# Kernel tuning notes

Hardware: AMD Instinct MI355X
Metric: run time of the kernel (lower is better)

Reference implementation:

```python
import jax, jax.numpy as jnp
import numpy as np

B, K, DIM, T_FRAMES = 4, 200, 256, 800

def _conv1d_same(x, w, b):
    # x: [B, K, Cin], w: [3, Cin, Cout] (WIO), 'same' padding over token axis
    y = jax.lax.conv_general_dilated(x, w, window_strides=(1,), padding='SAME',
                                     dimension_numbers=('NWC', 'WIO', 'NWC'))
    return y + b

def _swish_block(x, w1, b1, w2, b2):
    x = jax.nn.silu(x @ w1 + b1)
    return jax.nn.silu(x @ w2 + b2)

def setup_inputs() -> dict:
    key = jax.random.key(0)
    ks = jax.random.split(key, 10)
    def lin(k, fan_in, shape):
        return jax.random.normal(k, shape, dtype=jnp.float32) / np.sqrt(fan_in)
    inp = {
        'T': T_FRAMES,
        'durations': jax.random.uniform(ks[0], (B, K), dtype=jnp.float32) * 4.0,
        'features': jax.random.normal(ks[1], (B, K, DIM), dtype=jnp.float32),
        'conv1_w': lin(ks[2], 3 * DIM, (3, DIM, 8)),
        'conv1_b': jnp.zeros((8,), jnp.float32),
        'conv2_w': lin(ks[3], 3 * DIM, (3, DIM, 8)),
        'conv2_b': jnp.zeros((8,), jnp.float32),
        'sw1_w1': lin(ks[4], 10, (10, 16)), 'sw1_b1': jnp.zeros((16,), jnp.float32),
        'sw1_w2': lin(ks[5], 16, (16, 16)), 'sw1_b2': jnp.zeros((16,), jnp.float32),
        'sw2_w1': lin(ks[6], 10, (10, 2)), 'sw2_b1': jnp.zeros((2,), jnp.float32),
        'sw2_w2': lin(ks[7], 2, (2, 2)), 'sw2_b2': jnp.zeros((2,), jnp.float32),
        'p1_w': lin(ks[8], 2, (2, 1)), 'p1_b': jnp.zeros((1,), jnp.float32),
        'p2_w': lin(ks[9], 16, (16, DIM)), 'p2_b': jnp.zeros((DIM,), jnp.float32),
    }
    return inp

def reference(T, durations, features, conv1_w, conv1_b, conv2_w, conv2_b,
              sw1_w1, sw1_b1, sw1_w2, sw1_b2, sw2_w1, sw2_b1, sw2_w2, sw2_b2,
              p1_w, p1_b, p2_w, p2_b):
    # Conv + SiLU token feature extraction: [B, K, 8]
    left = jax.nn.silu(_conv1d_same(features, conv1_w, conv1_b))
    right = jax.nn.silu(_conv1d_same(features, conv2_w, conv2_b))
    # Token boundary grids S, E: [B, T, K]
    token_end = jnp.cumsum(durations, axis=1)          # [B, K]
    token_start = token_end - durations                # [B, K]
    t = jnp.arange(T, dtype=features.dtype)            # frame index grid
    S = t[None, :, None] - token_start[:, None, :]     # [B, T, K]
    E = token_end[:, None, :] - t[None, :, None]       # [B, T, K]
    Bn, Tn, Kn = S.shape
    # Concat (S, E, conv_feats) -> [B, T, K, 10]
    xleft = jnp.concatenate([S[..., None], E[..., None],
                             jnp.broadcast_to(left[:, None], (Bn, Tn, Kn, 8))], axis=-1)
    xright = jnp.concatenate([S[..., None], E[..., None],
                              jnp.broadcast_to(right[:, None], (Bn, Tn, Kn, 8))], axis=-1)
    C = _swish_block(xleft, sw1_w1, sw1_b1, sw1_w2, sw1_b2)      # [B, T, K, 16]
    r = _swish_block(xright, sw2_w1, sw2_b1, sw2_w2, sw2_b2)     # [B, T, K, 2]
    logits = (r @ p1_w + p1_b)[..., 0]                           # [B, T, K]
    W = jax.nn.softmax(logits, axis=-1)                          # attention over tokens
    # Upsampled output: weighted token features + projected auxiliary context
    O = jnp.einsum('btk,bkd->btd', W, features)
    A = jnp.einsum('btk,btkp->btp', W, C)                        # [B, T, 16]
    return O + (A @ p2_w + p2_b)
```

## Files before the change

### kernel.cpp

```cpp
#include <hip/hip_runtime.h>
#include <math.h>

#define B_   4
#define K_   200
#define DIM_ 256
#define T_   800
#define TT_  4

__device__ __forceinline__ float silu_f(float x) {
    return x / (1.0f + __expf(-x));
}

__global__ __launch_bounds__(64) void prep_kernel(
        const float* __restrict__ dur,
        const float* __restrict__ feats,
        const float* __restrict__ c1w, const float* __restrict__ c1b,
        const float* __restrict__ c2w, const float* __restrict__ c2b,
        float* __restrict__ starts, float* __restrict__ ends,
        float* __restrict__ left,   float* __restrict__ right) {
    const int b = blockIdx.y, chunk = blockIdx.x, k0 = chunk * 4;
    const int tid = threadIdx.x;

    __shared__ float wT[16][772];
    __shared__ float fT[6][260];

    for (int i = tid; i < 3 * DIM_ * 8; i += 64) {
        int tc = i >> 3, o = i & 7;
        wT[o][tc]     = c1w[i];
        wT[8 + o][tc] = c2w[i];
    }
    const float4* f4 = (const float4*)feats;
    for (int i = tid; i < 6 * 64; i += 64) {
        int r = i >> 6, c4 = i & 63;
        int kk = k0 - 1 + r;
        float4 v = make_float4(0.f, 0.f, 0.f, 0.f);
        if (kk >= 0 && kk < K_) v = f4[(b * K_ + kk) * 64 + c4];
        *(float4*)&fT[r][c4 * 4] = v;
    }
    __syncthreads();

    const int k = tid >> 4, oc = tid & 15, cv = oc >> 3, o = oc & 7;
    float acc = 0.f;
#pragma unroll
    for (int tap = 0; tap < 3; ++tap) {
#pragma unroll 8
        for (int c = 0; c < DIM_; c += 4) {
            float4 fv = *(const float4*)&fT[k + tap][c];
            float4 wv = *(const float4*)&wT[oc][tap * DIM_ + c];
            acc += fv.x * wv.x + fv.y * wv.y + fv.z * wv.z + fv.w * wv.w;
        }
    }
    int kk = k0 + k;
    if (kk < K_) {
        float bias = cv ? c2b[o] : c1b[o];
        float* dst = cv ? right : left;
        dst[(b * K_ + kk) * 8 + o] = silu_f(acc + bias);
    }

    if (chunk == 0) {
        float4 dv = make_float4(0.f, 0.f, 0.f, 0.f);
        if (tid < 50) dv = *(const float4*)&dur[b * K_ + tid * 4];
        float s0 = dv.x, s1 = s0 + dv.y, s2 = s1 + dv.z, s3 = s2 + dv.w;
        float sc = s3;
#pragma unroll
        for (int off = 1; off < 64; off <<= 1) {
            float v = __shfl_up(sc, off);
            if (tid >= off) sc += v;
        }
        float excl = sc - s3;
        if (tid < 50) {
            float4 st = make_float4(excl, excl + s0, excl + s1, excl + s2);
            float4 en = make_float4(excl + s0, excl + s1, excl + s2, excl + s3);
            *(float4*)&starts[b * K_ + tid * 4] = st;
            *(float4*)&ends  [b * K_ + tid * 4] = en;
        }
    }
}

__global__ __launch_bounds__(256) void main_kernel(
        const float* __restrict__ feats,
        const float* __restrict__ starts, const float* __restrict__ ends,
        const float* __restrict__ left,   const float* __restrict__ right,
        const float* __restrict__ sw1_w1, const float* __restrict__ sw1_b1,
        const float* __restrict__ sw1_w2, const float* __restrict__ sw1_b2,
        const float* __restrict__ sw2_w1, const float* __restrict__ sw2_b1,
        const float* __restrict__ sw2_w2, const float* __restrict__ sw2_b2,
        const float* __restrict__ p1_w,   const float* __restrict__ p1_b,
        const float* __restrict__ p2_w,   const float* __restrict__ p2_b,
        float* __restrict__ out) {
    const int t0 = blockIdx.x * TT_, b = blockIdx.y;
    const int tid = threadIdx.x, w = tid >> 6, l = tid & 63;
    const int t = t0 + w;

    __shared__ float sS[K_], sE[K_];
    __shared__ float upool[4096];
    __shared__ float W4[K_][4];
    __shared__ float At[16][4];
    __shared__ float lw1T[16][12];
    __shared__ float lw2T[16][16];
    __shared__ float lb1s[16], lb2s[16];

    for (int i = tid; i < K_; i += 256) { sS[i] = starts[b * K_ + i]; sE[i] = ends[b * K_ + i]; }
    const float4* L4 = (const float4*)(left  + b * K_ * 8);
    const float4* R4 = (const float4*)(right + b * K_ * 8);
    for (int j = tid; j < 2 * K_; j += 256) {
        int k = j >> 1, h = j & 1;
        *(float4*)&upool[k * 20 + h * 4]     = L4[j];
        *(float4*)&upool[k * 20 + 8 + h * 4] = R4[j];
    }
    for (int i = tid; i < 160; i += 256) lw1T[i & 15][i >> 4] = sw1_w1[i];
    if (tid < 16) { lw1T[tid][10] = 0.f; lw1T[tid][11] = 0.f; }
    lw2T[tid & 15][tid >> 4] = sw1_w2[tid];
    if (tid < 16) { lb1s[tid] = sw1_b1[tid]; lb2s[tid] = sw1_b2[tid]; }
    __syncthreads();

    float rw1[20];
#pragma unroll
    for (int i = 0; i < 20; ++i) rw1[i] = sw2_w1[i];
    const float rb10 = sw2_b1[0], rb11 = sw2_b1[1];
    const float rw20 = sw2_w2[0], rw21 = sw2_w2[1], rw22 = sw2_w2[2], rw23 = sw2_w2[3];
    const float rb20 = sw2_b2[0], rb21 = sw2_b2[1];
    const float p10 = p1_w[0], p11 = p1_w[1], p1b0 = p1_b[0];

    float Sv[4], Ev[4], lg[4], fL[4][8];
#pragma unroll
    for (int i = 0; i < 4; ++i) {
        int k = l + 64 * i;
        int kc = (k < K_) ? k : (K_ - 1);
        float S = (float)t - sS[kc];
        float E = sE[kc] - (float)t;
        Sv[i] = S; Ev[i] = E;
        float4 fa = *(const float4*)&upool[kc * 20];
        float4 fb = *(const float4*)&upool[kc * 20 + 4];
        fL[i][0] = fa.x; fL[i][1] = fa.y; fL[i][2] = fa.z; fL[i][3] = fa.w;
        fL[i][4] = fb.x; fL[i][5] = fb.y; fL[i][6] = fb.z; fL[i][7] = fb.w;
        float4 ra = *(const float4*)&upool[kc * 20 + 8];
        float4 rb = *(const float4*)&upool[kc * 20 + 12];
        float h0 = rb10 + S * rw1[0] + E * rw1[2]
                 + ra.x * rw1[4]  + ra.y * rw1[6]  + ra.z * rw1[8]  + ra.w * rw1[10]
                 + rb.x * rw1[12] + rb.y * rw1[14] + rb.z * rw1[16] + rb.w * rw1[18];
        float h1 = rb11 + S * rw1[1] + E * rw1[3]
                 + ra.x * rw1[5]  + ra.y * rw1[7]  + ra.z * rw1[9]  + ra.w * rw1[11]
                 + rb.x * rw1[13] + rb.y * rw1[15] + rb.z * rw1[17] + rb.w * rw1[19];
        h0 = silu_f(h0); h1 = silu_f(h1);
        float g0 = silu_f(rb20 + h0 * rw20 + h1 * rw22);
        float g1 = silu_f(rb21 + h0 * rw21 + h1 * rw23);
        lg[i] = (k < K_) ? (g0 * p10 + g1 * p11 + p1b0) : -1e30f;
    }

    float m = fmaxf(fmaxf(lg[0], lg[1]), fmaxf(lg[2], lg[3]));
#pragma unroll
    for (int off = 32; off > 0; off >>= 1) m = fmaxf(m, __shfl_xor(m, off));
    float e0 = __expf(lg[0] - m), e1 = __expf(lg[1] - m);
    float e2 = __expf(lg[2] - m), e3 = __expf(lg[3] - m);
    float ssum = e0 + e1 + e2 + e3;
#pragma unroll
    for (int off = 32; off > 0; off >>= 1) ssum += __shfl_xor(ssum, off);
    float inv = 1.0f / ssum;
    float wgt[4] = { e0 * inv, e1 * inv, e2 * inv, e3 * inv };
#pragma unroll
    for (int i = 0; i < 4; ++i) { int k = l + 64 * i; if (k < K_) W4[k][w] = wgt[i]; }

    float hmat[4][16];
#pragma unroll
    for (int j = 0; j < 16; ++j) {
        float4 wa = *(const float4*)&lw1T[j][0];
        float4 wb = *(const float4*)&lw1T[j][4];
        float4 wc = *(const float4*)&lw1T[j][8];
        float bj = lb1s[j];
#pragma unroll
        for (int i = 0; i < 4; ++i) {
            float a = bj + Sv[i] * wa.x + Ev[i] * wa.y
                    + fL[i][0] * wa.z + fL[i][1] * wa.w
                    + fL[i][2] * wb.x + fL[i][3] * wb.y
                    + fL[i][4] * wb.z + fL[i][5] * wb.w
                    + fL[i][6] * wc.x + fL[i][7] * wc.y;
            hmat[i][j] = silu_f(a);
        }
    }
    float acc[16];
#pragma unroll
    for (int j = 0; j < 16; ++j) {
        float4 w0 = *(const float4*)&lw2T[j][0];
        float4 w1v = *(const float4*)&lw2T[j][4];
        float4 w2v = *(const float4*)&lw2T[j][8];
        float4 w3v = *(const float4*)&lw2T[j][12];
        float bj = lb2s[j];
        float s = 0.f;
#pragma unroll
        for (int i = 0; i < 4; ++i) {
            float c = bj
                + hmat[i][0]  * w0.x  + hmat[i][1]  * w0.y  + hmat[i][2]  * w0.z  + hmat[i][3]  * w0.w
                + hmat[i][4]  * w1v.x + hmat[i][5]  * w1v.y + hmat[i][6]  * w1v.z + hmat[i][7]  * w1v.w
                + hmat[i][8]  * w2v.x + hmat[i][9]  * w2v.y + hmat[i][10] * w2v.z + hmat[i][11] * w2v.w
                + hmat[i][12] * w3v.x + hmat[i][13] * w3v.y + hmat[i][14] * w3v.z + hmat[i][15] * w3v.w;
            s += wgt[i] * silu_f(c);
        }
        acc[j] = s;
    }

    __syncthreads();
#pragma unroll
    for (int j = 0; j < 16; ++j) upool[(w * 16 + j) * 64 + l] = acc[j];
    __syncthreads();
    {
        int rwv = tid >> 6, rj = (tid >> 2) & 15, rq = tid & 3;
        const float* base = &upool[(rwv * 16 + rj) * 64 + rq * 16];
        float4 a0 = *(const float4*)&base[0];
        float4 a1 = *(const float4*)&base[4];
        float4 a2 = *(const float4*)&base[8];
        float4 a3 = *(const float4*)&base[12];
        float s = a0.x + a0.y + a0.z + a0.w + a1.x + a1.y + a1.z + a1.w
                + a2.x + a2.y + a2.z + a2.w + a3.x + a3.y + a3.z + a3.w;
        s += __shfl_down(s, 1);
        s += __shfl_down(s, 2);
        if (rq == 0) At[rj][rwv] = s;
    }
    __syncthreads();

    const float* fp = feats + (size_t)(b * K_) * DIM_ + tid;
    float o0 = 0.f, o1 = 0.f, o2 = 0.f, o3 = 0.f;
#pragma unroll 4
    for (int k = 0; k < K_; ++k) {
        float4 wv = *(const float4*)&W4[k][0];
        float f = fp[(size_t)k * DIM_];
        o0 += wv.x * f; o1 += wv.y * f; o2 += wv.z * f; o3 += wv.w * f;
    }
    float ab = p2_b[tid];
    float a0 = ab, a1 = ab, a2 = ab, a3 = ab;
#pragma unroll
    for (int p = 0; p < 16; ++p) {
        float pw = p2_w[p * DIM_ + tid];
        float4 av = *(const float4*)&At[p][0];
        a0 += av.x * pw; a1 += av.y * pw; a2 += av.z * pw; a3 += av.w * pw;
    }
    float* op = out + ((size_t)b * T_ + t0) * DIM_ + tid;
    op[0 * DIM_] = o0 + a0;
    op[1 * DIM_] = o1 + a1;
    op[2 * DIM_] = o2 + a2;
    op[3 * DIM_] = o3 + a3;
}

extern "C" void kernel_launch(void* const* d_in, const int* in_sizes, int n_in,
                              void* d_out, int out_size, void* d_ws, size_t ws_size,
                              hipStream_t stream) {
    const float* durations = (const float*)d_in[1];
    const float* features  = (const float*)d_in[2];
    const float* conv1_w   = (const float*)d_in[3];
    const float* conv1_b   = (const float*)d_in[4];
    const float* conv2_w   = (const float*)d_in[5];
    const float* conv2_b   = (const float*)d_in[6];
    const float* sw1_w1    = (const float*)d_in[7];
    const float* sw1_b1    = (const float*)d_in[8];
    const float* sw1_w2    = (const float*)d_in[9];
    const float* sw1_b2    = (const float*)d_in[10];
    const float* sw2_w1    = (const float*)d_in[11];
    const float* sw2_b1    = (const float*)d_in[12];
    const float* sw2_w2    = (const float*)d_in[13];
    const float* sw2_b2    = (const float*)d_in[14];
    const float* p1_w      = (const float*)d_in[15];
    const float* p1_b      = (const float*)d_in[16];
    const float* p2_w      = (const float*)d_in[17];
    const float* p2_b      = (const float*)d_in[18];
    float* out = (float*)d_out;

    float* ws     = (float*)d_ws;
    float* starts = ws;
    float* ends   = starts + B_ * K_;
    float* left   = ends + B_ * K_;
    float* right  = left + B_ * K_ * 8;

    prep_kernel<<<dim3(50, B_), 64, 0, stream>>>(
        durations, features, conv1_w, conv1_b, conv2_w, conv2_b,
        starts, ends, left, right);
    main_kernel<<<dim3(T_ / TT_, B_), 256, 0, stream>>>(
        features, starts, ends, left, right,
        sw1_w1, sw1_b1, sw1_w2, sw1_b2,
        sw2_w1, sw2_b1, sw2_w2, sw2_b2,
        p1_w, p1_b, p2_w, p2_b, out);
}
```

Baseline: 148.3 us.

## Precompute per-token first-layer affine terms and split feature GEMV across waves

The first linear layer of both swish blocks is algebraically split: since S = t - start and E = end - t, the token-dependent part (bias, conv features, start/end terms) is precomputed per token in the prep kernel. The main kernel then adds only a per-frame scalar times (w_S - w_E) instead of a 10-wide dot product per (t,k). The weighted feature sum is also restructured so each wave covers 50 tokens with float4 feature loads, followed by a shared-memory reduction, and the reduction buffer is padded to avoid bank conflicts. The prep kernel now reads conv inputs directly from global memory with fewer, larger blocks.

```diff
diff --git a/kernel.cpp b/kernel.cpp
--- a/kernel.cpp
+++ b/kernel.cpp
@@ -5,59 +5,37 @@
 #define K_   200
 #define DIM_ 256
 #define T_   800
-#define TT_  4
+
+#define S_UP 68
 
 __device__ __forceinline__ float silu_f(float x) {
     return x / (1.0f + __expf(-x));
 }
 
-__global__ __launch_bounds__(64) void prep_kernel(
+__global__ __launch_bounds__(256) void prep_kernel(
         const float* __restrict__ dur,
         const float* __restrict__ feats,
         const float* __restrict__ c1w, const float* __restrict__ c1b,
         const float* __restrict__ c2w, const float* __restrict__ c2b,
-        float* __restrict__ starts, float* __restrict__ ends,
-        float* __restrict__ left,   float* __restrict__ right) {
-    const int b = blockIdx.y, chunk = blockIdx.x, k0 = chunk * 4;
-    const int tid = threadIdx.x;
-
-    __shared__ float wT[16][772];
-    __shared__ float fT[6][260];
-
-    for (int i = tid; i < 3 * DIM_ * 8; i += 64) {
+        const float* __restrict__ sw1_w1, const float* __restrict__ sw1_b1,
+        const float* __restrict__ sw2_w1, const float* __restrict__ sw2_b1,
+        float* __restrict__ cw) {
+    const int b = blockIdx.y, k0 = blockIdx.x * 16;
+    const int tid = threadIdx.x, w = tid >> 6, l = tid & 63;
+
+    __shared__ float wT[16][769];
+    __shared__ float sSc[K_], sEc[K_];
+    __shared__ float sfeat[16][16];
+
+    for (int i = tid; i < 3 * DIM_ * 8; i += 256) {
         int tc = i >> 3, o = i & 7;
-        wT[o][tc]     = c1w[i];
+        wT[o][tc] = c1w[i];
+    }
+    for (int i = tid; i < 3 * DIM_ * 8; i += 256) {
+        int tc = i >> 3, o = i & 7;
         wT[8 + o][tc] = c2w[i];
     }
-    const float4* f4 = (const float4*)feats;
-    for (int i = tid; i < 6 * 64; i += 64) {
-        int r = i >> 6, c4 = i & 63;
-        int kk = k0 - 1 + r;
-        float4 v = make_float4(0.f, 0.f, 0.f, 0.f);
-        if (kk >= 0 && kk < K_) v = f4[(b * K_ + kk) * 64 + c4];
-        *(float4*)&fT[r][c4 * 4] = v;
-    }
-    __syncthreads();
-
-    const int k = tid >> 4, oc = tid & 15, cv = oc >> 3, o = oc & 7;
-    float acc = 0.f;
-#pragma unroll
-    for (int tap = 0; tap < 3; ++tap) {
-#pragma unroll 8
-        for (int c = 0; c < DIM_; c += 4) {
-            float4 fv = *(const float4*)&fT[k + tap][c];
-            float4 wv = *(const float4*)&wT[oc][tap * DIM_ + c];
-            acc += fv.x * wv.x + fv.y * wv.y + fv.z * wv.z + fv.w * wv.w;
-        }
-    }
-    int kk = k0 + k;
-    if (kk < K_) {
-        float bias = cv ? c2b[o] : c1b[o];
-        float* dst = cv ? right : left;
-        dst[(b * K_ + kk) * 8 + o] = silu_f(acc + bias);
-    }
-
-    if (chunk == 0) {
+    if (tid < 64) {
         float4 dv = make_float4(0.f, 0.f, 0.f, 0.f);
         if (tid < 50) dv = *(const float4*)&dur[b * K_ + tid * 4];
         float s0 = dv.x, s1 = s0 + dv.y, s2 = s1 + dv.z, s3 = s2 + dv.w;
@@ -69,85 +47,107 @@
         }
         float excl = sc - s3;
         if (tid < 50) {
-            float4 st = make_float4(excl, excl + s0, excl + s1, excl + s2);
-            float4 en = make_float4(excl + s0, excl + s1, excl + s2, excl + s3);
-            *(float4*)&starts[b * K_ + tid * 4] = st;
-            *(float4*)&ends  [b * K_ + tid * 4] = en;
+            *(float4*)&sSc[tid * 4] = make_float4(excl, excl + s0, excl + s1, excl + s2);
+            *(float4*)&sEc[tid * 4] = make_float4(excl + s0, excl + s1, excl + s2, excl + s3);
+        }
+    }
+    __syncthreads();
+
+    const int kl = w * 4 + (l >> 4);
+    const int k  = k0 + kl;
+    const int oc = l & 15, o = oc & 7;
+    const float4* f4 = (const float4*)feats;
+    float acc = 0.f;
+#pragma unroll
+    for (int tap = 0; tap < 3; ++tap) {
+        int kk = k + tap - 1;
+        bool valid = (kk >= 0 && kk < K_);
+        int kc = valid ? kk : 0;
+        const float4* fr = f4 + (size_t)(b * K_ + kc) * 64;
+        float tacc = 0.f;
+#pragma unroll 8
+        for (int c4 = 0; c4 < 64; ++c4) {
+            float4 fv = fr[c4];
+            float4 wv = *(const float4*)&wT[oc][tap * DIM_ + c4 * 4];
+            tacc += fv.x * wv.x + fv.y * wv.y + fv.z * wv.z + fv.w * wv.w;
+        }
+        acc += valid ? tacc : 0.f;
+    }
+    float bias = (oc < 8) ? c1b[o] : c2b[o];
+    sfeat[kl][oc] = silu_f(acc + bias);
+    __syncthreads();
+
+    {
+        const int j = tid >> 4, klc = tid & 15;
+        const int kk = k0 + klc;
+        if (kk < K_) {
+            float st = sSc[kk], en = sEc[kk];
+            float a = sw1_b1[j] - st * sw1_w1[j] + en * sw1_w1[16 + j];
+#pragma unroll
+            for (int i = 0; i < 8; ++i) a += sfeat[klc][i] * sw1_w1[(2 + i) * 16 + j];
+            cw[(b * 18 + 2 + j) * K_ + kk] = a;
+        }
+    }
+    if (tid < 32) {
+        const int which = tid >> 4, klc = tid & 15;
+        const int kk = k0 + klc;
+        if (kk < K_) {
+            float st = sSc[kk], en = sEc[kk];
+            float a = sw2_b1[which] - st * sw2_w1[which] + en * sw2_w1[2 + which];
+#pragma unroll
+            for (int i = 0; i < 8; ++i) a += sfeat[klc][8 + i] * sw2_w1[(2 + i) * 2 + which];
+            cw[(b * 18 + which) * K_ + kk] = a;
         }
     }
 }
 
 __global__ __launch_bounds__(256) void main_kernel(
         const float* __restrict__ feats,
-        const float* __restrict__ starts, const float* __restrict__ ends,
-        const float* __restrict__ left,   const float* __restrict__ right,
-        const float* __restrict__ sw1_w1, const float* __restrict__ sw1_b1,
-        const float* __restrict__ sw1_w2, const float* __restrict__ sw1_b2,
-        const float* __restrict__ sw2_w1, const float* __restrict__ sw2_b1,
-        const float* __restrict__ sw2_w2, const float* __restrict__ sw2_b2,
+        const float* __restrict__ cw,
+        const float* __restrict__ sw1_w1, const float* __restrict__ sw1_w2,
+        const float* __restrict__ sw1_b2,
+        const float* __restrict__ sw2_w1, const float* __restrict__ sw2_w2,
+        const float* __restrict__ sw2_b2,
         const float* __restrict__ p1_w,   const float* __restrict__ p1_b,
         const float* __restrict__ p2_w,   const float* __restrict__ p2_b,
         float* __restrict__ out) {
-    const int t0 = blockIdx.x * TT_, b = blockIdx.y;
+    const int t0 = blockIdx.x * 4, b = blockIdx.y;
     const int tid = threadIdx.x, w = tid >> 6, l = tid & 63;
     const int t = t0 + w;
 
-    __shared__ float sS[K_], sE[K_];
-    __shared__ float upool[4096];
-    __shared__ float W4[K_][4];
-    __shared__ float At[16][4];
-    __shared__ float lw1T[16][12];
+    __shared__ alignas(16) float cb[18 * K_];
+    __shared__ alignas(16) float upool[64 * S_UP];
+    __shared__ alignas(16) float W4[K_][4];
+    __shared__ alignas(16) float At[16][4];
     __shared__ float lw2T[16][16];
-    __shared__ float lb1s[16], lb2s[16];
-
-    for (int i = tid; i < K_; i += 256) { sS[i] = starts[b * K_ + i]; sE[i] = ends[b * K_ + i]; }
-    const float4* L4 = (const float4*)(left  + b * K_ * 8);
-    const float4* R4 = (const float4*)(right + b * K_ * 8);
-    for (int j = tid; j < 2 * K_; j += 256) {
-        int k = j >> 1, h = j & 1;
-        *(float4*)&upool[k * 20 + h * 4]     = L4[j];
-        *(float4*)&upool[k * 20 + 8 + h * 4] = R4[j];
-    }
-    for (int i = tid; i < 160; i += 256) lw1T[i & 15][i >> 4] = sw1_w1[i];
-    if (tid < 16) { lw1T[tid][10] = 0.f; lw1T[tid][11] = 0.f; }
+    __shared__ float lb2s[16];
+
+    {
+        const float4* cg4 = (const float4*)(cw + b * 18 * K_);
+        float4* cb4 = (float4*)cb;
+        for (int i = tid; i < 18 * K_ / 4; i += 256) cb4[i] = cg4[i];
+    }
     lw2T[tid & 15][tid >> 4] = sw1_w2[tid];
-    if (tid < 16) { lb1s[tid] = sw1_b1[tid]; lb2s[tid] = sw1_b2[tid]; }
-    __syncthreads();
-
-    float rw1[20];
-#pragma unroll
-    for (int i = 0; i < 20; ++i) rw1[i] = sw2_w1[i];
-    const float rb10 = sw2_b1[0], rb11 = sw2_b1[1];
+    if (tid < 16) lb2s[tid] = sw1_b2[tid];
+    __syncthreads();
+
+    const float tf = (float)t;
+    const float a0 = sw2_w1[0] - sw2_w1[2], a1 = sw2_w1[1] - sw2_w1[3];
     const float rw20 = sw2_w2[0], rw21 = sw2_w2[1], rw22 = sw2_w2[2], rw23 = sw2_w2[3];
     const float rb20 = sw2_b2[0], rb21 = sw2_b2[1];
     const float p10 = p1_w[0], p11 = p1_w[1], p1b0 = p1_b[0];
 
-    float Sv[4], Ev[4], lg[4], fL[4][8];
+    float lg[4];
 #pragma unroll
     for (int i = 0; i < 4; ++i) {
         int k = l + 64 * i;
         int kc = (k < K_) ? k : (K_ - 1);
-        float S = (float)t - sS[kc];
-        float E = sE[kc] - (float)t;
-        Sv[i] = S; Ev[i] = E;
-        float4 fa = *(const float4*)&upool[kc * 20];
-        float4 fb = *(const float4*)&upool[kc * 20 + 4];
-        fL[i][0] = fa.x; fL[i][1] = fa.y; fL[i][2] = fa.z; fL[i][3] = fa.w;
-        fL[i][4] = fb.x; fL[i][5] = fb.y; fL[i][6] = fb.z; fL[i][7] = fb.w;
-        float4 ra = *(const float4*)&upool[kc * 20 + 8];
-        float4 rb = *(const float4*)&upool[kc * 20 + 12];
-        float h0 = rb10 + S * rw1[0] + E * rw1[2]
-                 + ra.x * rw1[4]  + ra.y * rw1[6]  + ra.z * rw1[8]  + ra.w * rw1[10]
-                 + rb.x * rw1[12] + rb.y * rw1[14] + rb.z * rw1[16] + rb.w * rw1[18];
-        float h1 = rb11 + S * rw1[1] + E * rw1[3]
-                 + ra.x * rw1[5]  + ra.y * rw1[7]  + ra.z * rw1[9]  + ra.w * rw1[11]
-                 + rb.x * rw1[13] + rb.y * rw1[15] + rb.z * rw1[17] + rb.w * rw1[19];
-        h0 = silu_f(h0); h1 = silu_f(h1);
+        float h0 = silu_f(fmaf(a0, tf, cb[0 * K_ + kc]));
+        float h1 = silu_f(fmaf(a1, tf, cb[1 * K_ + kc]));
         float g0 = silu_f(rb20 + h0 * rw20 + h1 * rw22);
         float g1 = silu_f(rb21 + h0 * rw21 + h1 * rw23);
         lg[i] = (k < K_) ? (g0 * p10 + g1 * p11 + p1b0) : -1e30f;
     }
-
     float m = fmaxf(fmaxf(lg[0], lg[1]), fmaxf(lg[2], lg[3]));
 #pragma unroll
     for (int off = 32; off > 0; off >>= 1) m = fmaxf(m, __shfl_xor(m, off));
@@ -161,21 +161,18 @@
 #pragma unroll
     for (int i = 0; i < 4; ++i) { int k = l + 64 * i; if (k < K_) W4[k][w] = wgt[i]; }
 
+    float ajt[16];
+#pragma unroll
+    for (int j = 0; j < 16; ++j) ajt[j] = (sw1_w1[j] - sw1_w1[16 + j]) * tf;
+
     float hmat[4][16];
 #pragma unroll
     for (int j = 0; j < 16; ++j) {
-        float4 wa = *(const float4*)&lw1T[j][0];
-        float4 wb = *(const float4*)&lw1T[j][4];
-        float4 wc = *(const float4*)&lw1T[j][8];
-        float bj = lb1s[j];
 #pragma unroll
         for (int i = 0; i < 4; ++i) {
-            float a = bj + Sv[i] * wa.x + Ev[i] * wa.y
-                    + fL[i][0] * wa.z + fL[i][1] * wa.w
-                    + fL[i][2] * wb.x + fL[i][3] * wb.y
-                    + fL[i][4] * wb.z + fL[i][5] * wb.w
-                    + fL[i][6] * wc.x + fL[i][7] * wc.y;
-            hmat[i][j] = silu_f(a);
+            int k = l + 64 * i;
+            int kc = (k < K_) ? k : (K_ - 1);
+            hmat[i][j] = silu_f(ajt[j] + cb[(2 + j) * K_ + kc]);
         }
     }
     float acc[16];
@@ -199,46 +196,73 @@
         acc[j] = s;
     }
 
-    __syncthreads();
-#pragma unroll
-    for (int j = 0; j < 16; ++j) upool[(w * 16 + j) * 64 + l] = acc[j];
+#pragma unroll
+    for (int j = 0; j < 16; ++j) upool[(w * 16 + j) * S_UP + l] = acc[j];
     __syncthreads();
     {
         int rwv = tid >> 6, rj = (tid >> 2) & 15, rq = tid & 3;
-        const float* base = &upool[(rwv * 16 + rj) * 64 + rq * 16];
-        float4 a0 = *(const float4*)&base[0];
-        float4 a1 = *(const float4*)&base[4];
-        float4 a2 = *(const float4*)&base[8];
-        float4 a3 = *(const float4*)&base[12];
-        float s = a0.x + a0.y + a0.z + a0.w + a1.x + a1.y + a1.z + a1.w
-                + a2.x + a2.y + a2.z + a2.w + a3.x + a3.y + a3.z + a3.w;
+        const float* base = &upool[(rwv * 16 + rj) * S_UP + rq * 16];
+        float4 b0 = *(const float4*)&base[0];
+        float4 b1 = *(const float4*)&base[4];
+        float4 b2 = *(const float4*)&base[8];
+        float4 b3 = *(const float4*)&base[12];
+        float s = b0.x + b0.y + b0.z + b0.w + b1.x + b1.y + b1.z + b1.w
+                + b2.x + b2.y + b2.z + b2.w + b3.x + b3.y + b3.z + b3.w;
         s += __shfl_down(s, 1);
         s += __shfl_down(s, 2);
         if (rq == 0) At[rj][rwv] = s;
     }
     __syncthreads();
 
-    const float* fp = feats + (size_t)(b * K_) * DIM_ + tid;
-    float o0 = 0.f, o1 = 0.f, o2 = 0.f, o3 = 0.f;
-#pragma unroll 4
-    for (int k = 0; k < K_; ++k) {
-        float4 wv = *(const float4*)&W4[k][0];
-        float f = fp[(size_t)k * DIM_];
-        o0 += wv.x * f; o1 += wv.y * f; o2 += wv.z * f; o3 += wv.w * f;
-    }
-    float ab = p2_b[tid];
-    float a0 = ab, a1 = ab, a2 = ab, a3 = ab;
-#pragma unroll
-    for (int p = 0; p < 16; ++p) {
-        float pw = p2_w[p * DIM_ + tid];
-        float4 av = *(const float4*)&At[p][0];
-        a0 += av.x * pw; a1 += av.y * pw; a2 += av.z * pw; a3 += av.w * pw;
-    }
-    float* op = out + ((size_t)b * T_ + t0) * DIM_ + tid;
-    op[0 * DIM_] = o0 + a0;
-    op[1 * DIM_] = o1 + a1;
-    op[2 * DIM_] = o2 + a2;
-    op[3 * DIM_] = o3 + a3;
+    {
+        const float4* fB4 = (const float4*)(feats + (size_t)b * K_ * DIM_);
+        float4 po[4];
+#pragma unroll
+        for (int f = 0; f < 4; ++f) po[f] = make_float4(0.f, 0.f, 0.f, 0.f);
+        const int kb = w * 50;
+        for (int kk = 0; kk < 50; ++kk) {
+            int k = kb + kk;
+            float4 wv = *(const float4*)&W4[k][0];
+            float4 fv = fB4[k * 64 + l];
+            po[0].x += wv.x * fv.x; po[0].y += wv.x * fv.y; po[0].z += wv.x * fv.z; po[0].w += wv.x * fv.w;
+            po[1].x += wv.y * fv.x; po[1].y += wv.y * fv.y; po[1].z += wv.y * fv.z; po[1].w += wv.y * fv.w;
+            po[2].x += wv.z * fv.x; po[2].y += wv.z * fv.y; po[2].z += wv.z * fv.z; po[2].w += wv.z * fv.w;
+            po[3].x += wv.w * fv.x; po[3].y += wv.w * fv.y; po[3].z += wv.w * fv.z; po[3].w += wv.w * fv.w;
+        }
+#pragma unroll
+        for (int f = 0; f < 4; ++f) {
+            upool[(w * 16 + f * 4 + 0) * S_UP + l] = po[f].x;
+            upool[(w * 16 + f * 4 + 1) * S_UP + l] = po[f].y;
+            upool[(w * 16 + f * 4 + 2) * S_UP + l] = po[f].z;
+            upool[(w * 16 + f * 4 + 3) * S_UP + l] = po[f].w;
+        }
+    }
+    __syncthreads();
+
+    {
+        const int d = tid, l0 = d >> 2, q = d & 3;
+        float v0 = 0.f, v1 = 0.f, v2 = 0.f, v3 = 0.f;
+#pragma unroll
+        for (int ww = 0; ww < 4; ++ww) {
+            v0 += upool[(ww * 16 + 0 * 4 + q) * S_UP + l0];
+            v1 += upool[(ww * 16 + 1 * 4 + q) * S_UP + l0];
+            v2 += upool[(ww * 16 + 2 * 4 + q) * S_UP + l0];
+            v3 += upool[(ww * 16 + 3 * 4 + q) * S_UP + l0];
+        }
+        float ab = p2_b[d];
+        v0 += ab; v1 += ab; v2 += ab; v3 += ab;
+#pragma unroll
+        for (int p = 0; p < 16; ++p) {
+            float pw = p2_w[p * DIM_ + d];
+            float4 av = *(const float4*)&At[p][0];
+            v0 += av.x * pw; v1 += av.y * pw; v2 += av.z * pw; v3 += av.w * pw;
+        }
+        float* op = out + ((size_t)b * T_ + t0) * DIM_ + d;
+        op[0 * DIM_] = v0;
+        op[1 * DIM_] = v1;
+        op[2 * DIM_] = v2;
+        op[3 * DIM_] = v3;
+    }
 }
 
 extern "C" void kernel_launch(void* const* d_in, const int* in_sizes, int n_in,
@@ -264,18 +288,14 @@
     const float* p2_b      = (const float*)d_in[18];
     float* out = (float*)d_out;
 
-    float* ws     = (float*)d_ws;
-    float* starts = ws;
-    float* ends   = starts + B_ * K_;
-    float* left   = ends + B_ * K_;
-    float* right  = left + B_ * K_ * 8;
-
-    prep_kernel<<<dim3(50, B_), 64, 0, stream>>>(
+    float* cw = (float*)d_ws;
+
+    prep_kernel<<<dim3(13, B_), 256, 0, stream>>>(
         durations, features, conv1_w, conv1_b, conv2_w, conv2_b,
-        starts, ends, left, right);
-    main_kernel<<<dim3(T_ / TT_, B_), 256, 0, stream>>>(
-        features, starts, ends, left, right,
-        sw1_w1, sw1_b1, sw1_w2, sw1_b2,
-        sw2_w1, sw2_b1, sw2_w2, sw2_b2,
+        sw1_w1, sw1_b1, sw2_w1, sw2_b1, cw);
+    main_kernel<<<dim3(T_ / 4, B_), 256, 0, stream>>>(
+        features, cw,
+        sw1_w1, sw1_w2, sw1_b2,
+        sw2_w1, sw2_w2, sw2_b2,
         p1_w, p1_b, p2_w, p2_b, out);
 }
```

New measurement: 140.2 us. 1.06x faster.
